# Optimization experiments

Measured on AMD Instinct MI355X. Metric: run time of the kernel, lower is better.

The kernel has to match this reference:

```python
import jax, jax.numpy as jnp
import numpy as np

B, S, D, H, G = 4, 2048, 1024, 16, 32
HD = D // H
LN_EPS = 1e-5


def _lin_init(key, fan_in, fan_out):
    kw, kb = jax.random.split(key)
    bound = 1.0 / np.sqrt(fan_in)
    W = jax.random.uniform(kw, (fan_in, fan_out), jnp.float32, -bound, bound)
    b = jax.random.uniform(kb, (fan_out,), jnp.float32, -bound, bound)
    return W, b


def setup_inputs() -> dict:
    key = jax.random.key(0)
    ks = jax.random.split(key, 9)
    x = jax.random.normal(ks[0], (B, S, D), jnp.float32)
    geo_features = jax.random.normal(ks[1], (B, G), jnp.float32)
    Wq, bq = _lin_init(ks[2], D, D)
    Wk, bk = _lin_init(ks[3], D, D)
    Wv, bv = _lin_init(ks[4], D, D)
    Wo, bo = _lin_init(ks[5], D, D)
    ge_W1, ge_b1 = _lin_init(ks[6], G, D)
    ln_g = jnp.ones((D,), jnp.float32)
    ln_b = jnp.zeros((D,), jnp.float32)
    ge_W2, ge_b2 = _lin_init(ks[7], D, D)
    gm_W, gm_b = _lin_init(ks[8], D, H)
    return dict(x=x, geo_features=geo_features, Wq=Wq, bq=bq, Wk=Wk, bk=bk,
                Wv=Wv, bv=bv, Wo=Wo, bo=bo, ge_W1=ge_W1, ge_b1=ge_b1,
                ln_g=ln_g, ln_b=ln_b, ge_W2=ge_W2, ge_b2=ge_b2,
                gm_W=gm_W, gm_b=gm_b)


def reference(x, geo_features, Wq, bq, Wk, bk, Wv, bv, Wo, bo,
              ge_W1, ge_b1, ln_g, ln_b, ge_W2, ge_b2, gm_W, gm_b):
    # QKV projections -> (B, H, S, HD)
    def split_heads(t):
        return t.reshape(B, S, H, HD).transpose(0, 2, 1, 3)
    Q = split_heads(x @ Wq + bq)
    K = split_heads(x @ Wk + bk)
    V = split_heads(x @ Wv + bv)

    # geo encoder: Linear -> LayerNorm -> ReLU -> Linear
    h = geo_features @ ge_W1 + ge_b1                      # (B, D)
    mu = jnp.mean(h, axis=-1, keepdims=True)
    var = jnp.mean(jnp.square(h - mu), axis=-1, keepdims=True)
    h = (h - mu) / jnp.sqrt(var + LN_EPS) * ln_g + ln_b
    h = jax.nn.relu(h)
    geo_encoded = h @ ge_W2 + ge_b2                       # (B, D)
    geo_mod = jax.nn.sigmoid(geo_encoded @ gm_W + gm_b)   # (B, H)

    scale = 1.0 / np.sqrt(HD)
    scores = jnp.einsum('bhqd,bhkd->bhqk', Q, K) * scale  # (B, H, S, S)
    scores = scores * (1.0 + geo_mod[:, :, None, None])
    attn = jax.nn.softmax(scores, axis=-1)                # dropout in eval mode: identity
    ctx = jnp.einsum('bhqk,bhkd->bhqd', attn, V)          # (B, H, S, HD)
    ctx = ctx.transpose(0, 2, 1, 3).reshape(B, S, D)
    out = ctx @ Wo + bo
    return out, attn
```

## Files before the change

kernel.cpp:

```cpp
#include <hip/hip_runtime.h>

typedef __attribute__((ext_vector_type(8))) short bf16x8;
typedef __attribute__((ext_vector_type(4))) float f32x4;
typedef __attribute__((ext_vector_type(4))) unsigned short us4;
typedef unsigned short u16;

#define MB (1024*1024)

#define WAITV(N) asm volatile("s_waitcnt vmcnt(" #N ")" ::: "memory")
#define WAITL0() asm volatile("s_waitcnt lgkmcnt(0)" ::: "memory")
#define BAR()    __builtin_amdgcn_s_barrier()
#define SCHEDB() __builtin_amdgcn_sched_barrier(0)

__device__ __forceinline__ u16 f2bf(float f) {
    unsigned u = __float_as_uint(f);
    unsigned r = (u + 0x7fffu + ((u >> 16) & 1u)) >> 16;
    return (u16)r;
}

__device__ __forceinline__ unsigned cvtpk(float a, float b) {
    unsigned r;
    asm("v_cvt_pk_bf16_f32 %0, %1, %2" : "=v"(r) : "v"(a), "v"(b));
    return r;
}

__device__ __forceinline__ f32x4 mfma16(bf16x8 a, bf16x8 b, f32x4 c) {
    return __builtin_amdgcn_mfma_f32_16x16x32_bf16(a, b, c, 0, 0, 0);
}

__device__ __forceinline__ void gload16(const void* g, void* l) {
    __builtin_amdgcn_global_load_lds(
        (__attribute__((address_space(1))) void*)(unsigned long long)g,
        (__attribute__((address_space(3))) void*)l, 16, 0, 0);
}

__global__ __launch_bounds__(256) void k_cvtx(const float* __restrict__ x, u16* __restrict__ xb) {
    const long long i = (long long)blockIdx.x * 256 + threadIdx.x;
    const float4* xp = (const float4*)x;
    float4 a = xp[i*2], b = xp[i*2+1];
    bf16x8 o;
    o[0]=(short)f2bf(a.x); o[1]=(short)f2bf(a.y); o[2]=(short)f2bf(a.z); o[3]=(short)f2bf(a.w);
    o[4]=(short)f2bf(b.x); o[5]=(short)f2bf(b.y); o[6]=(short)f2bf(b.z); o[7]=(short)f2bf(b.w);
    *(bf16x8*)&xb[i*8] = o;
}

__global__ __launch_bounds__(256) void k_wtcvt(const float* __restrict__ W0, const float* __restrict__ W1,
                                               const float* __restrict__ W2, const float* __restrict__ W3,
                                               u16* __restrict__ wt) {
    __shared__ float tl[32][33];
    const int t = threadIdx.x, z = blockIdx.z;
    const float* W = (z==0)?W0:(z==1)?W1:(z==2)?W2:W3;
    const int k0 = blockIdx.x*32, n0 = blockIdx.y*32;
    const int r = t >> 3, c4 = (t & 7) * 4;
    float4 v = *(const float4*)&W[(long long)(k0+r)*1024 + n0 + c4];
    tl[r][c4] = v.x; tl[r][c4+1] = v.y; tl[r][c4+2] = v.z; tl[r][c4+3] = v.w;
    __syncthreads();
    us4 ov;
    ov[0] = f2bf(tl[c4+0][r]); ov[1] = f2bf(tl[c4+1][r]);
    ov[2] = f2bf(tl[c4+2][r]); ov[3] = f2bf(tl[c4+3][r]);
    *(us4*)&wt[((long long)z << 20) + (long long)(n0+r)*1024 + k0 + c4] = ov;
}

__global__ __launch_bounds__(1024) void k_geo(const float* __restrict__ geo, const float* __restrict__ W1,
                                              const float* __restrict__ b1, const float* __restrict__ lng,
                                              const float* __restrict__ lnb, const float* __restrict__ W2,
                                              const float* __restrict__ b2, const float* __restrict__ gmW,
                                              const float* __restrict__ gmb, float* __restrict__ qs) {
    const int b = blockIdx.x, j = threadIdx.x;
    __shared__ float hs[1024];
    __shared__ float ges[1024];
    __shared__ float parts[64][16];
    __shared__ float r1[16], r2[16];
    __shared__ float mu_s, rv_s;

    float acc = b1[j];
    #pragma unroll 8
    for (int g = 0; g < 32; ++g) acc += geo[b*32+g] * W1[(long long)g*1024 + j];
    float s1 = acc, s2 = acc*acc;
    #pragma unroll
    for (int m = 1; m < 64; m <<= 1) { s1 += __shfl_xor(s1, m); s2 += __shfl_xor(s2, m); }
    const int wid = j >> 6, lid = j & 63;
    if (lid == 0) { r1[wid] = s1; r2[wid] = s2; }
    __syncthreads();
    if (j == 0) {
        float S1 = 0.f, S2 = 0.f;
        for (int i = 0; i < 16; ++i) { S1 += r1[i]; S2 += r2[i]; }
        float mu = S1 / 1024.f;
        float var = S2 / 1024.f - mu*mu;
        mu_s = mu; rv_s = rsqrtf(var + 1e-5f);
    }
    __syncthreads();
    float hv = (acc - mu_s) * rv_s * lng[j] + lnb[j];
    hs[j] = fmaxf(hv, 0.f);
    __syncthreads();

    float acc2 = b2[j];
    #pragma unroll 8
    for (int d = 0; d < 1024; ++d) acc2 += hs[d] * W2[(long long)d*1024 + j];
    ges[j] = acc2;
    __syncthreads();

    const int hh = j & 15, seg = j >> 4;
    float part = 0.f;
    #pragma unroll
    for (int dd = 0; dd < 16; ++dd) {
        const int d = seg*16 + dd;
        part += ges[d] * gmW[d*16 + hh];
    }
    parts[seg][hh] = part;
    __syncthreads();
    if (j < 16) {
        float s = gmb[j];
        for (int k = 0; k < 64; ++k) s += parts[k][j];
        qs[b*16 + j] = 0.125f * (1.f + 1.f/(1.f + __expf(-s)));
    }
}

__global__ __launch_bounds__(256) void k_qkv_gemm(const u16* __restrict__ xb, const u16* __restrict__ wtq,
                                                  const float* __restrict__ bq, const float* __restrict__ bk,
                                                  const float* __restrict__ bv, u16* __restrict__ outq) {
    __shared__ u16 lA[128*64];
    __shared__ u16 lB[128*64];
    const int t = threadIdx.x, z = blockIdx.z;
    const int m0 = blockIdx.y * 128, n0 = blockIdx.x * 128;
    const u16* wt = wtq + (long long)z * (1024*1024);
    const float* bias = (z==0) ? bq : (z==1) ? bk : bv;
    u16* out = outq + (long long)z * 8388608;
    const int w = t >> 6, l = t & 63, lm = l & 15, lg = l >> 4;
    const int wr = (w >> 1) * 64, wc = (w & 1) * 64;
    f32x4 acc[4][4] = {};
    const char* gA = (const char*)xb + (long long)(m0 + (t>>3))*2048 + (t&7)*16;
    const char* gB = (const char*)wt + (long long)(n0 + (t>>3))*2048 + (t&7)*16;
    char* lAp = (char*)lA + t*16;
    char* lBp = (char*)lB + t*16;
    for (int k0 = 0; k0 < 1024; k0 += 64) {
        #pragma unroll
        for (int i = 0; i < 4; ++i) {
            gload16(gA + (long long)i*32*2048, lAp + i*4096);
            gload16(gB + (long long)i*32*2048, lBp + i*4096);
        }
        gA += 128; gB += 128;
        __syncthreads();
        #pragma unroll
        for (int kk = 0; kk < 2; ++kk) {
            bf16x8 af[4], bfr[4];
            #pragma unroll
            for (int mi = 0; mi < 4; ++mi)
                af[mi] = *(const bf16x8*)((const char*)lA + (wr + mi*16 + lm)*128 + kk*64 + lg*16);
            #pragma unroll
            for (int ni = 0; ni < 4; ++ni)
                bfr[ni] = *(const bf16x8*)((const char*)lB + (wc + ni*16 + lm)*128 + kk*64 + lg*16);
            #pragma unroll
            for (int mi = 0; mi < 4; ++mi)
                #pragma unroll
                for (int ni = 0; ni < 4; ++ni)
                    acc[mi][ni] = mfma16(bfr[ni], af[mi], acc[mi][ni]);
        }
        __syncthreads();
    }
    #pragma unroll
    for (int mi = 0; mi < 4; ++mi) {
        const int m = m0 + wr + mi*16 + lm;
        const int b = m >> 11, s = m & 2047;
        #pragma unroll
        for (int ni = 0; ni < 4; ++ni) {
            const int nb = n0 + wc + ni*16 + lg*4;
            const float4 bn4 = *(const float4*)&bias[nb];
            const int hh = nb >> 6, d = nb & 63;
            uint2 pk;
            pk.x = cvtpk(acc[mi][ni][0] + bn4.x, acc[mi][ni][1] + bn4.y);
            pk.y = cvtpk(acc[mi][ni][2] + bn4.z, acc[mi][ni][3] + bn4.w);
            *(uint2*)&out[(((long long)b*16 + hh)*2048 + s)*64 + d] = pk;
        }
    }
}

__global__ __launch_bounds__(256) void k_vtrans(const u16* __restrict__ vb, u16* __restrict__ vt) {
    __shared__ u16 tl[64][40];
    const int t = threadIdx.x;
    const int bh = blockIdx.z, s0 = blockIdx.y*64, d0 = blockIdx.x*32;
    const u16* vsrc = vb + (long long)bh*2048*64;
    {
        const int sl = t >> 2, dg = t & 3;
        bf16x8 v = *(const bf16x8*)&vsrc[(long long)(s0+sl)*64 + d0 + dg*8];
        *(bf16x8*)&tl[sl][dg*8] = v;
    }
    __syncthreads();
    {
        const int dl = t >> 3, sg = t & 7;
        bf16x8 o;
        #pragma unroll
        for (int j = 0; j < 8; ++j) o[j] = (short)tl[sg*8+j][dl];
        *(bf16x8*)&vt[((long long)bh*64 + d0+dl)*2048 + s0 + sg*8] = o;
    }
}

__global__ __launch_bounds__(512, 4) void k_attn(const u16* __restrict__ Qb, const u16* __restrict__ Kb,
                                                 const u16* __restrict__ Vt, const float* __restrict__ qsv,
                                                 float* __restrict__ attn_out, u16* __restrict__ ctxb) {
    __shared__ char lds[65536];

    const int nl = blockIdx.x;
    const int ob = (nl & 7)*64 + (nl >> 3);
    const int bh = ob >> 3, qt = ob & 7;
    const int t = threadIdx.x, w = t >> 6, l = t & 63, lm = l & 15, lg = l >> 4;
    const int q0 = qt * 256;
    const float qs = qsv[bh];

    const char* KB = (const char*)Kb + (long long)bh * 262144;
    const char* VB = (const char*)Vt + (long long)bh * 262144;

    bf16x8 qf[2][2];
    {
        const char* QB = (const char*)Qb + (long long)bh * 262144;
        #pragma unroll
        for (int ms = 0; ms < 2; ++ms)
            #pragma unroll
            for (int kc = 0; kc < 2; ++kc)
                qf[ms][kc] = *(const bf16x8*)(QB + (long long)(q0 + w*32 + ms*16 + lm)*128 + kc*64 + lg*16);
    }

    const int off = t*16;
    const int row = off >> 7, cb = off & 127;
    const int offA = off;
    const int srcK = row*128  + (cb ^ ((row & 7) << 4));
    const int srcV = row*4096 + (cb ^ ((row & 7) << 4));

    float lsum[2] = {0.f, 0.f};
    {
        gload16(KB + srcK, lds + offA);
        gload16(KB + 8192 + srcK, lds + 8192 + offA);
        SCHEDB();
        WAITV(1); BAR(); SCHEDB();

        int cb_ = 0, sb_ = 2;
        for (int kt = 0; kt < 32; ++kt) {
            const int ktn = (kt < 30) ? kt + 2 : 31;
            gload16(KB + (long long)ktn*8192 + srcK, lds + sb_*8192 + offA);
            SCHEDB();
            const char* kb = lds + cb_*8192;
            #pragma unroll
            for (int ns = 0; ns < 4; ++ns) {
                const int rowb = ns*16 + lm;
                const int tag = (rowb & 7) << 4;
                bf16x8 kf0 = *(const bf16x8*)(kb + rowb*128 + ((lg*16) ^ tag));
                bf16x8 kf1 = *(const bf16x8*)(kb + rowb*128 + ((64 + lg*16) ^ tag));
                #pragma unroll
                for (int ms = 0; ms < 2; ++ms) {
                    f32x4 a = {};
                    a = mfma16(kf0, qf[ms][0], a);
                    a = mfma16(kf1, qf[ms][1], a);
                    lsum[ms] += __expf(a[0]*qs) + __expf(a[1]*qs)
                              + __expf(a[2]*qs) + __expf(a[3]*qs);
                }
            }
            WAITV(1); BAR(); SCHEDB();
            cb_ = (cb_ == 2) ? 0 : cb_ + 1;
            sb_ = (sb_ == 2) ? 0 : sb_ + 1;
        }
    }
    WAITV(0); BAR(); SCHEDB();

    float invl[2];
    #pragma unroll
    for (int ms = 0; ms < 2; ++ms) {
        float v = lsum[ms];
        v += __shfl_xor(v, 16);
        v += __shfl_xor(v, 32);
        invl[ms] = 1.f / v;
    }

    char* lP = lds + 32768;
    float* aL = attn_out + ((long long)bh*2048 + q0 + w*32 + lm)*2048 + lg*4;
    f32x4 cacc[2][4] = {};

    {
        gload16(KB + srcK, lds + offA);
        gload16(VB + srcV, lds + 16384 + offA);
        SCHEDB();
        WAITV(0); BAR(); SCHEDB();

        for (int kt = 0; kt < 32; ++kt) {
            const int cur = kt & 1, nxt = cur ^ 1;
            const int ktn = (kt < 31) ? kt + 1 : 31;
            gload16(KB + (long long)ktn*8192 + srcK, lds + nxt*8192 + offA);
            gload16(VB + (long long)ktn*128 + srcV, lds + 16384 + nxt*8192 + offA);
            SCHEDB();

            const char* kb = lds + cur*8192;
            #pragma unroll
            for (int ns = 0; ns < 4; ++ns) {
                const int rowb = ns*16 + lm;
                const int tag = (rowb & 7) << 4;
                bf16x8 kf0 = *(const bf16x8*)(kb + rowb*128 + ((lg*16) ^ tag));
                bf16x8 kf1 = *(const bf16x8*)(kb + rowb*128 + ((64 + lg*16) ^ tag));
                #pragma unroll
                for (int ms = 0; ms < 2; ++ms) {
                    f32x4 a = {};
                    a = mfma16(kf0, qf[ms][0], a);
                    a = mfma16(kf1, qf[ms][1], a);
                    const float p0 = __expf(a[0]*qs) * invl[ms];
                    const float p1 = __expf(a[1]*qs) * invl[ms];
                    const float p2 = __expf(a[2]*qs) * invl[ms];
                    const float p3 = __expf(a[3]*qs) * invl[ms];
                    f32x4 pv4 = {p0, p1, p2, p3};
                    *(f32x4*)(aL + ms*32768 + kt*64 + ns*16) = pv4;
                    const int prow = w*32 + ms*16 + lm;
                    const int ptag = (prow & 7) << 4;
                    uint2 pk; pk.x = cvtpk(p0, p1); pk.y = cvtpk(p2, p3);
                    *(uint2*)(lP + prow*128 + ((32*ns + 8*lg) ^ ptag)) = pk;
                }
            }
            WAITL0(); SCHEDB();

            const char* vb = lds + 16384 + cur*8192;
            #pragma unroll
            for (int ks = 0; ks < 2; ++ks) {
                bf16x8 pa[2];
                #pragma unroll
                for (int ms = 0; ms < 2; ++ms) {
                    const int prow = w*32 + ms*16 + lm;
                    pa[ms] = *(const bf16x8*)(lP + prow*128 + ((ks*64 + lg*16) ^ ((prow & 7) << 4)));
                }
                #pragma unroll
                for (int dn = 0; dn < 4; ++dn) {
                    const int rv = dn*16 + lm;
                    bf16x8 vf = *(const bf16x8*)(vb + rv*128 + ((ks*64 + lg*16) ^ ((rv & 7) << 4)));
                    cacc[0][dn] = mfma16(pa[0], vf, cacc[0][dn]);
                    cacc[1][dn] = mfma16(pa[1], vf, cacc[1][dn]);
                }
            }
            WAITV(8); BAR(); SCHEDB();
        }
    }

    const int b = bh >> 4, hh = bh & 15;
    #pragma unroll
    for (int ms = 0; ms < 2; ++ms)
        #pragma unroll
        for (int dn = 0; dn < 4; ++dn)
            #pragma unroll
            for (int r = 0; r < 4; ++r) {
                const int q = q0 + w*32 + ms*16 + lg*4 + r;
                ctxb[(((long long)b*2048 + q)*16 + hh)*64 + dn*16 + lm] = f2bf(cacc[ms][dn][r]);
            }
}

__global__ __launch_bounds__(256) void k_o_gemm(const u16* __restrict__ ab, const u16* __restrict__ wt,
                                                const float* __restrict__ bo, float* __restrict__ outf) {
    __shared__ u16 lA[128*64];
    __shared__ u16 lB[128*64];
    const int t = threadIdx.x;
    const int m0 = blockIdx.y * 128, n0 = blockIdx.x * 128;
    const int w = t >> 6, l = t & 63, lm = l & 15, lg = l >> 4;
    const int wr = (w >> 1) * 64, wc = (w & 1) * 64;
    f32x4 acc[4][4] = {};
    const char* gA = (const char*)ab + (long long)(m0 + (t>>3))*2048 + (t&7)*16;
    const char* gB = (const char*)wt + (long long)(n0 + (t>>3))*2048 + (t&7)*16;
    char* lAp = (char*)lA + t*16;
    char* lBp = (char*)lB + t*16;
    for (int k0 = 0; k0 < 1024; k0 += 64) {
        #pragma unroll
        for (int i = 0; i < 4; ++i) {
            gload16(gA + (long long)i*32*2048, lAp + i*4096);
            gload16(gB + (long long)i*32*2048, lBp + i*4096);
        }
        gA += 128; gB += 128;
        __syncthreads();
        #pragma unroll
        for (int kk = 0; kk < 2; ++kk) {
            bf16x8 af[4], bfr[4];
            #pragma unroll
            for (int mi = 0; mi < 4; ++mi)
                af[mi] = *(const bf16x8*)((const char*)lA + (wr + mi*16 + lm)*128 + kk*64 + lg*16);
            #pragma unroll
            for (int ni = 0; ni < 4; ++ni)
                bfr[ni] = *(const bf16x8*)((const char*)lB + (wc + ni*16 + lm)*128 + kk*64 + lg*16);
            #pragma unroll
            for (int mi = 0; mi < 4; ++mi)
                #pragma unroll
                for (int ni = 0; ni < 4; ++ni)
                    acc[mi][ni] = mfma16(bfr[ni], af[mi], acc[mi][ni]);
        }
        __syncthreads();
    }
    #pragma unroll
    for (int mi = 0; mi < 4; ++mi) {
        const int m = m0 + wr + mi*16 + lm;
        #pragma unroll
        for (int ni = 0; ni < 4; ++ni) {
            const int nb = n0 + wc + ni*16 + lg*4;
            const float4 bn4 = *(const float4*)&bo[nb];
            f32x4 v = acc[mi][ni];
            v[0] += bn4.x; v[1] += bn4.y; v[2] += bn4.z; v[3] += bn4.w;
            *(f32x4*)&outf[(long long)m*1024 + nb] = v;
        }
    }
}

extern "C" void kernel_launch(void* const* d_in, const int* in_sizes, int n_in,
                              void* d_out, int out_size, void* d_ws, size_t ws_size,
                              hipStream_t stream) {
    const float* x    = (const float*)d_in[0];
    const float* geo  = (const float*)d_in[1];
    const float* Wq   = (const float*)d_in[2];
    const float* bq   = (const float*)d_in[3];
    const float* Wk   = (const float*)d_in[4];
    const float* bk   = (const float*)d_in[5];
    const float* Wv   = (const float*)d_in[6];
    const float* bv   = (const float*)d_in[7];
    const float* Wo   = (const float*)d_in[8];
    const float* bo   = (const float*)d_in[9];
    const float* geW1 = (const float*)d_in[10];
    const float* geb1 = (const float*)d_in[11];
    const float* lng  = (const float*)d_in[12];
    const float* lnb  = (const float*)d_in[13];
    const float* geW2 = (const float*)d_in[14];
    const float* geb2 = (const float*)d_in[15];
    const float* gmW  = (const float*)d_in[16];
    const float* gmb  = (const float*)d_in[17];

    char* ws = (char*)d_ws;
    u16* xb   = (u16*)(ws + 0);
    u16* wt   = (u16*)(ws + 16*(size_t)MB);
    u16* qkv  = (u16*)(ws + 24*(size_t)MB);
    u16* Qb   = qkv;
    u16* Kb   = (u16*)(ws + 40*(size_t)MB);
    u16* Vb   = (u16*)(ws + 56*(size_t)MB);
    u16* Vt   = (u16*)(ws + 72*(size_t)MB);
    u16* ctx  = Vb;
    float* qsb= (float*)(ws + 88*(size_t)MB);

    float* outf = (float*)d_out;
    float* attn = outf + 8388608;

    hipLaunchKernelGGL(k_cvtx,    dim3(4096),      dim3(256),  0, stream, x, xb);
    hipLaunchKernelGGL(k_wtcvt,   dim3(32,32,4),   dim3(256),  0, stream, Wq, Wk, Wv, Wo, wt);
    hipLaunchKernelGGL(k_geo,     dim3(4),         dim3(1024), 0, stream, geo, geW1, geb1, lng, lnb, geW2, geb2, gmW, gmb, qsb);
    hipLaunchKernelGGL(k_qkv_gemm,dim3(8,64,3),    dim3(256),  0, stream, xb, wt, bq, bk, bv, qkv);
    hipLaunchKernelGGL(k_vtrans,  dim3(2,32,64),   dim3(256),  0, stream, Vb, Vt);
    hipLaunchKernelGGL(k_attn,    dim3(512),       dim3(512),  0, stream, Qb, Kb, Vt, qsb, attn, ctx);
    hipLaunchKernelGGL(k_o_gemm,  dim3(8,64),      dim3(256),  0, stream, ctx, wt + 3*1048576, bo, outf);
}
```

Before: 595.9 us.

## Split attention into fused single-pass ctx kernel and separate probability-write kernel

```diff
diff --git a/kernel.cpp b/kernel.cpp
--- a/kernel.cpp
+++ b/kernel.cpp
@@ -195,10 +195,10 @@
     }
 }
 
-__global__ __launch_bounds__(512, 4) void k_attn(const u16* __restrict__ Qb, const u16* __restrict__ Kb,
-                                                 const u16* __restrict__ Vt, const float* __restrict__ qsv,
-                                                 float* __restrict__ attn_out, u16* __restrict__ ctxb) {
-    __shared__ char lds[65536];
+__global__ __launch_bounds__(512, 4) void k_attn_ctx(const u16* __restrict__ Qb, const u16* __restrict__ Kb,
+                                                     const u16* __restrict__ Vt, const float* __restrict__ qsv,
+                                                     float* __restrict__ invg, u16* __restrict__ ctxb) {
+    __shared__ char lds[81920];
 
     const int nl = blockIdx.x;
     const int ob = (nl & 7)*64 + (nl >> 3);
@@ -221,45 +221,75 @@
     }
 
     const int off = t*16;
-    const int row = off >> 7, cb = off & 127;
+    const int row = off >> 7, cbyt = off & 127;
     const int offA = off;
-    const int srcK = row*128  + (cb ^ ((row & 7) << 4));
-    const int srcV = row*4096 + (cb ^ ((row & 7) << 4));
-
+    const int srcK = row*128  + (cbyt ^ ((row & 7) << 4));
+    const int srcV = row*4096 + (cbyt ^ ((row & 7) << 4));
+
+    char* lP = lds + 49152;
     float lsum[2] = {0.f, 0.f};
-    {
-        gload16(KB + srcK, lds + offA);
-        gload16(KB + 8192 + srcK, lds + 8192 + offA);
+    f32x4 cacc[2][4] = {};
+
+    gload16(KB + srcK, lds + offA);
+    gload16(VB + srcV, lds + 24576 + offA);
+    gload16(KB + 8192 + srcK, lds + 8192 + offA);
+    gload16(VB + 128 + srcV, lds + 24576 + 8192 + offA);
+    SCHEDB();
+    WAITV(2); BAR(); SCHEDB();
+
+    int cb_ = 0, sb_ = 2;
+    for (int kt = 0; kt < 32; ++kt) {
+        const int ktn = (kt < 30) ? kt + 2 : 31;
+        gload16(KB + (long long)ktn*8192 + srcK, lds + sb_*8192 + offA);
+        gload16(VB + (long long)ktn*128 + srcV, lds + 24576 + sb_*8192 + offA);
         SCHEDB();
-        WAITV(1); BAR(); SCHEDB();
-
-        int cb_ = 0, sb_ = 2;
-        for (int kt = 0; kt < 32; ++kt) {
-            const int ktn = (kt < 30) ? kt + 2 : 31;
-            gload16(KB + (long long)ktn*8192 + srcK, lds + sb_*8192 + offA);
-            SCHEDB();
-            const char* kb = lds + cb_*8192;
-            #pragma unroll
-            for (int ns = 0; ns < 4; ++ns) {
-                const int rowb = ns*16 + lm;
-                const int tag = (rowb & 7) << 4;
-                bf16x8 kf0 = *(const bf16x8*)(kb + rowb*128 + ((lg*16) ^ tag));
-                bf16x8 kf1 = *(const bf16x8*)(kb + rowb*128 + ((64 + lg*16) ^ tag));
-                #pragma unroll
-                for (int ms = 0; ms < 2; ++ms) {
-                    f32x4 a = {};
-                    a = mfma16(kf0, qf[ms][0], a);
-                    a = mfma16(kf1, qf[ms][1], a);
-                    lsum[ms] += __expf(a[0]*qs) + __expf(a[1]*qs)
-                              + __expf(a[2]*qs) + __expf(a[3]*qs);
-                }
+
+        const char* kb = lds + cb_*8192;
+        #pragma unroll
+        for (int ns = 0; ns < 4; ++ns) {
+            const int rowb = ns*16 + lm;
+            const int tag = (rowb & 7) << 4;
+            bf16x8 kf0 = *(const bf16x8*)(kb + rowb*128 + ((lg*16) ^ tag));
+            bf16x8 kf1 = *(const bf16x8*)(kb + rowb*128 + ((64 + lg*16) ^ tag));
+            #pragma unroll
+            for (int ms = 0; ms < 2; ++ms) {
+                f32x4 a = {};
+                a = mfma16(kf0, qf[ms][0], a);
+                a = mfma16(kf1, qf[ms][1], a);
+                const float p0 = __expf(a[0]*qs);
+                const float p1 = __expf(a[1]*qs);
+                const float p2 = __expf(a[2]*qs);
+                const float p3 = __expf(a[3]*qs);
+                lsum[ms] += (p0 + p1) + (p2 + p3);
+                const int prow = w*32 + ms*16 + lm;
+                const int ptag = (prow & 7) << 4;
+                uint2 pk; pk.x = cvtpk(p0, p1); pk.y = cvtpk(p2, p3);
+                *(uint2*)(lP + prow*128 + ((32*ns + 8*lg) ^ ptag)) = pk;
             }
-            WAITV(1); BAR(); SCHEDB();
-            cb_ = (cb_ == 2) ? 0 : cb_ + 1;
-            sb_ = (sb_ == 2) ? 0 : sb_ + 1;
-        }
-    }
-    WAITV(0); BAR(); SCHEDB();
+        }
+        WAITL0(); SCHEDB();
+
+        const char* vb = lds + 24576 + cb_*8192;
+        #pragma unroll
+        for (int ks = 0; ks < 2; ++ks) {
+            bf16x8 pa[2];
+            #pragma unroll
+            for (int ms = 0; ms < 2; ++ms) {
+                const int prow = w*32 + ms*16 + lm;
+                pa[ms] = *(const bf16x8*)(lP + prow*128 + ((ks*64 + lg*16) ^ ((prow & 7) << 4)));
+            }
+            #pragma unroll
+            for (int dn = 0; dn < 4; ++dn) {
+                const int rv = dn*16 + lm;
+                bf16x8 vf = *(const bf16x8*)(vb + rv*128 + ((ks*64 + lg*16) ^ ((rv & 7) << 4)));
+                cacc[0][dn] = mfma16(pa[0], vf, cacc[0][dn]);
+                cacc[1][dn] = mfma16(pa[1], vf, cacc[1][dn]);
+            }
+        }
+        WAITV(2); BAR(); SCHEDB();
+        cb_ = (cb_ == 2) ? 0 : cb_ + 1;
+        sb_ = (sb_ == 2) ? 0 : sb_ + 1;
+    }
 
     float invl[2];
     #pragma unroll
@@ -269,70 +299,16 @@
         v += __shfl_xor(v, 32);
         invl[ms] = 1.f / v;
     }
-
-    char* lP = lds + 32768;
-    float* aL = attn_out + ((long long)bh*2048 + q0 + w*32 + lm)*2048 + lg*4;
-    f32x4 cacc[2][4] = {};
-
-    {
-        gload16(KB + srcK, lds + offA);
-        gload16(VB + srcV, lds + 16384 + offA);
-        SCHEDB();
-        WAITV(0); BAR(); SCHEDB();
-
-        for (int kt = 0; kt < 32; ++kt) {
-            const int cur = kt & 1, nxt = cur ^ 1;
-            const int ktn = (kt < 31) ? kt + 1 : 31;
-            gload16(KB + (long long)ktn*8192 + srcK, lds + nxt*8192 + offA);
-            gload16(VB + (long long)ktn*128 + srcV, lds + 16384 + nxt*8192 + offA);
-            SCHEDB();
-
-            const char* kb = lds + cur*8192;
-            #pragma unroll
-            for (int ns = 0; ns < 4; ++ns) {
-                const int rowb = ns*16 + lm;
-                const int tag = (rowb & 7) << 4;
-                bf16x8 kf0 = *(const bf16x8*)(kb + rowb*128 + ((lg*16) ^ tag));
-                bf16x8 kf1 = *(const bf16x8*)(kb + rowb*128 + ((64 + lg*16) ^ tag));
-                #pragma unroll
-                for (int ms = 0; ms < 2; ++ms) {
-                    f32x4 a = {};
-                    a = mfma16(kf0, qf[ms][0], a);
-                    a = mfma16(kf1, qf[ms][1], a);
-                    const float p0 = __expf(a[0]*qs) * invl[ms];
-                    const float p1 = __expf(a[1]*qs) * invl[ms];
-                    const float p2 = __expf(a[2]*qs) * invl[ms];
-                    const float p3 = __expf(a[3]*qs) * invl[ms];
-                    f32x4 pv4 = {p0, p1, p2, p3};
-                    *(f32x4*)(aL + ms*32768 + kt*64 + ns*16) = pv4;
-                    const int prow = w*32 + ms*16 + lm;
-                    const int ptag = (prow & 7) << 4;
-                    uint2 pk; pk.x = cvtpk(p0, p1); pk.y = cvtpk(p2, p3);
-                    *(uint2*)(lP + prow*128 + ((32*ns + 8*lg) ^ ptag)) = pk;
-                }
-            }
-            WAITL0(); SCHEDB();
-
-            const char* vb = lds + 16384 + cur*8192;
-            #pragma unroll
-            for (int ks = 0; ks < 2; ++ks) {
-                bf16x8 pa[2];
-                #pragma unroll
-                for (int ms = 0; ms < 2; ++ms) {
-                    const int prow = w*32 + ms*16 + lm;
-                    pa[ms] = *(const bf16x8*)(lP + prow*128 + ((ks*64 + lg*16) ^ ((prow & 7) << 4)));
-                }
-                #pragma unroll
-                for (int dn = 0; dn < 4; ++dn) {
-                    const int rv = dn*16 + lm;
-                    bf16x8 vf = *(const bf16x8*)(vb + rv*128 + ((ks*64 + lg*16) ^ ((rv & 7) << 4)));
-                    cacc[0][dn] = mfma16(pa[0], vf, cacc[0][dn]);
-                    cacc[1][dn] = mfma16(pa[1], vf, cacc[1][dn]);
-                }
-            }
-            WAITV(8); BAR(); SCHEDB();
-        }
-    }
+    if (lg == 0) {
+        invg[bh*2048 + q0 + w*32 + lm]      = invl[0];
+        invg[bh*2048 + q0 + w*32 + 16 + lm] = invl[1];
+    }
+    float* fs = (float*)(lP + w*4096);
+    if (lg == 0) { fs[lm] = invl[0]; fs[16 + lm] = invl[1]; }
+    WAITL0(); SCHEDB();
+    f32x4 iv[2];
+    iv[0] = *(const f32x4*)&fs[lg*4];
+    iv[1] = *(const f32x4*)&fs[16 + lg*4];
 
     const int b = bh >> 4, hh = bh & 15;
     #pragma unroll
@@ -342,8 +318,92 @@
             #pragma unroll
             for (int r = 0; r < 4; ++r) {
                 const int q = q0 + w*32 + ms*16 + lg*4 + r;
-                ctxb[(((long long)b*2048 + q)*16 + hh)*64 + dn*16 + lm] = f2bf(cacc[ms][dn][r]);
+                ctxb[(((long long)b*2048 + q)*16 + hh)*64 + dn*16 + lm] = f2bf(cacc[ms][dn][r] * iv[ms][r]);
             }
+}
+
+__global__ __launch_bounds__(256, 4) void k_pwrite(const u16* __restrict__ Qb, const u16* __restrict__ Kb,
+                                                   const float* __restrict__ qsv, const float* __restrict__ invg,
+                                                   float* __restrict__ attn_out) {
+    __shared__ char lds[40960];
+
+    const int nl = blockIdx.x;
+    const int ob = (nl & 7)*128 + (nl >> 3);
+    const int bh = ob >> 4, qt = ob & 15;
+    const int t = threadIdx.x, w = t >> 6, l = t & 63, lm = l & 15, lg = l >> 4;
+    const int q0 = qt * 128;
+    const float qs = qsv[bh];
+
+    const char* KB = (const char*)Kb + (long long)bh * 262144;
+
+    bf16x8 qf[2][2];
+    {
+        const char* QB = (const char*)Qb + (long long)bh * 262144;
+        #pragma unroll
+        for (int ms = 0; ms < 2; ++ms)
+            #pragma unroll
+            for (int kc = 0; kc < 2; ++kc)
+                qf[ms][kc] = *(const bf16x8*)(QB + (long long)(q0 + w*32 + ms*16 + lm)*128 + kc*64 + lg*16);
+    }
+    float invq[2];
+    invq[0] = invg[bh*2048 + q0 + w*32 + lm];
+    invq[1] = invg[bh*2048 + q0 + w*32 + 16 + lm];
+
+    int offA[2], srcK[2];
+    #pragma unroll
+    for (int i = 0; i < 2; ++i) {
+        const int off = i*4096 + t*16;
+        const int row = off >> 7, cbyt = off & 127;
+        offA[i] = off;
+        srcK[i] = row*128 + (cbyt ^ ((row & 7) << 4));
+    }
+
+    float* aL = attn_out + ((long long)bh*2048 + q0 + w*32 + lm)*2048 + lg*4;
+
+    #pragma unroll
+    for (int tt = 0; tt < 4; ++tt)
+        #pragma unroll
+        for (int i = 0; i < 2; ++i)
+            gload16(KB + (long long)tt*8192 + srcK[i], lds + tt*8192 + offA[i]);
+    SCHEDB();
+    WAITV(6); BAR(); SCHEDB();
+
+    int cur = 0, nb = 4;
+    for (int kt = 0; kt < 32; ++kt) {
+        const int ktn = (kt < 28) ? kt + 4 : 31;
+        #pragma unroll
+        for (int i = 0; i < 2; ++i)
+            gload16(KB + (long long)ktn*8192 + srcK[i], lds + nb*8192 + offA[i]);
+        SCHEDB();
+
+        const char* kb = lds + cur*8192;
+        #pragma unroll
+        for (int ns = 0; ns < 4; ++ns) {
+            const int rowb = ns*16 + lm;
+            const int tag = (rowb & 7) << 4;
+            bf16x8 kf0 = *(const bf16x8*)(kb + rowb*128 + ((lg*16) ^ tag));
+            bf16x8 kf1 = *(const bf16x8*)(kb + rowb*128 + ((64 + lg*16) ^ tag));
+            #pragma unroll
+            for (int ms = 0; ms < 2; ++ms) {
+                f32x4 a = {};
+                a = mfma16(kf0, qf[ms][0], a);
+                a = mfma16(kf1, qf[ms][1], a);
+                f32x4 pv4;
+                pv4[0] = __expf(a[0]*qs) * invq[ms];
+                pv4[1] = __expf(a[1]*qs) * invq[ms];
+                pv4[2] = __expf(a[2]*qs) * invq[ms];
+                pv4[3] = __expf(a[3]*qs) * invq[ms];
+                *(f32x4*)(aL + ms*32768 + kt*64 + ns*16) = pv4;
+            }
+        }
+        if (kt == 0)      { WAITV(14); }
+        else if (kt == 1) { WAITV(22); }
+        else if (kt == 2) { WAITV(30); }
+        else              { WAITV(38); }
+        BAR(); SCHEDB();
+        cur = (cur == 4) ? 0 : cur + 1;
+        nb  = (nb  == 4) ? 0 : nb  + 1;
+    }
 }
 
 __global__ __launch_bounds__(256) void k_o_gemm(const u16* __restrict__ ab, const u16* __restrict__ wt,
@@ -430,15 +490,17 @@
     u16* Vt   = (u16*)(ws + 72*(size_t)MB);
     u16* ctx  = Vb;
     float* qsb= (float*)(ws + 88*(size_t)MB);
+    float* invg = (float*)(ws + 0);
 
     float* outf = (float*)d_out;
     float* attn = outf + 8388608;
 
-    hipLaunchKernelGGL(k_cvtx,    dim3(4096),      dim3(256),  0, stream, x, xb);
-    hipLaunchKernelGGL(k_wtcvt,   dim3(32,32,4),   dim3(256),  0, stream, Wq, Wk, Wv, Wo, wt);
-    hipLaunchKernelGGL(k_geo,     dim3(4),         dim3(1024), 0, stream, geo, geW1, geb1, lng, lnb, geW2, geb2, gmW, gmb, qsb);
-    hipLaunchKernelGGL(k_qkv_gemm,dim3(8,64,3),    dim3(256),  0, stream, xb, wt, bq, bk, bv, qkv);
-    hipLaunchKernelGGL(k_vtrans,  dim3(2,32,64),   dim3(256),  0, stream, Vb, Vt);
-    hipLaunchKernelGGL(k_attn,    dim3(512),       dim3(512),  0, stream, Qb, Kb, Vt, qsb, attn, ctx);
-    hipLaunchKernelGGL(k_o_gemm,  dim3(8,64),      dim3(256),  0, stream, ctx, wt + 3*1048576, bo, outf);
-}
+    hipLaunchKernelGGL(k_cvtx,     dim3(4096),      dim3(256),  0, stream, x, xb);
+    hipLaunchKernelGGL(k_wtcvt,    dim3(32,32,4),   dim3(256),  0, stream, Wq, Wk, Wv, Wo, wt);
+    hipLaunchKernelGGL(k_geo,      dim3(4),         dim3(1024), 0, stream, geo, geW1, geb1, lng, lnb, geW2, geb2, gmW, gmb, qsb);
+    hipLaunchKernelGGL(k_qkv_gemm, dim3(8,64,3),    dim3(256),  0, stream, xb, wt, bq, bk, bv, qkv);
+    hipLaunchKernelGGL(k_vtrans,   dim3(2,32,64),   dim3(256),  0, stream, Vb, Vt);
+    hipLaunchKernelGGL(k_attn_ctx, dim3(512),       dim3(512),  0, stream, Qb, Kb, Vt, qsb, invg, ctx);
+    hipLaunchKernelGGL(k_pwrite,   dim3(1024),      dim3(256),  0, stream, Qb, Kb, qsb, invg, attn);
+    hipLaunchKernelGGL(k_o_gemm,   dim3(8,64),      dim3(256),  0, stream, ctx, wt + 3*1048576, bo, outf);
+}
```

Result: slower. 613.3 us (+2.9%).
